# Kernel tuning notes

Measured on AMD Instinct MI355X. Metric: run time of the kernel, lower is better.

The kernel has to match this reference:

```python
import jax, jax.numpy as jnp
import numpy as np

B, N = 2, 6
FC, FH, FW = 256, 32, 88            # encoder feature shape
ORFH, ORFW = 256, 704               # original image H, W
OUT_C = 128
D_ST, D_END, D_STEP = 1.0, 60.0, 3.0
NXV, NYV, NZV = 256, 256, 1         # BEV voxel grid (x, y, z)
DXV = np.array([0.4, 0.4, 20.0], np.float32)          # dx
BXV = np.array([-51.0, -51.0, 0.0], np.float32)       # bx = bound_lo + dx/2
BN_EPS = 1e-3


def _conv(x, w, b):
    y = jax.lax.conv_general_dilated(x, w, (1, 1), 'SAME',
                                     dimension_numbers=('NCHW', 'OIHW', 'NCHW'))
    return y + b[None, :, None, None]


def _bn(x, scale, bias, mean, var):
    inv = scale / jnp.sqrt(var + BN_EPS)
    return x * inv[None, :, None, None] + (bias - mean * inv)[None, :, None, None]


def _frustum():
    ds = jnp.arange(D_ST, D_END, D_STEP, dtype=jnp.float32)      # (D,)
    xs = jnp.linspace(0.0, ORFW - 1.0, FW)
    ys = jnp.linspace(0.0, ORFH - 1.0, FH)
    f = jnp.stack(jnp.broadcast_arrays(xs[None, None, :], ys[None, :, None],
                                       ds[:, None, None]), axis=-1)  # (D,FH,FW,3)
    return f, ds


def _forward(cam2ego_rot, cam2ego_trans, cam_intrins, post_cam2ego_rot,
             post_cam2ego_trans, img_feats,
             conv1_w, conv1_b, bn1_s, bn1_b, bn1_m, bn1_v,
             conv2_w, conv2_b, bn2_s, bn2_b, bn2_m, bn2_v,
             conv3_w, conv3_b):
    frustum, depth_vals = _frustum()
    D = depth_vals.shape[0]
    # ---- geometry (GaussianLSS.get_geometry) ----
    pts = frustum[None, None] - post_cam2ego_trans[:, :, None, None, None, :]
    inv_post = jnp.linalg.inv(post_cam2ego_rot)                       # (B,N,3,3)
    pts = jnp.einsum('bnij,bndhwj->bndhwi', inv_post, pts)
    pts = jnp.concatenate([pts[..., :2] * pts[..., 2:3], pts[..., 2:3]], -1)
    combine = cam2ego_rot @ jnp.linalg.inv(cam_intrins)
    geometry = (jnp.einsum('bnij,bndhwj->bndhwi', combine, pts)
                + cam2ego_trans[:, :, None, None, None, :])           # (B,N,D,H,W,3)
    # ---- depth net + gaussian depth distribution (get_cam_feature) ----
    x = img_feats.reshape(B * N, FC, FH, FW)
    x = jax.nn.relu(_bn(_conv(x, conv1_w, conv1_b), bn1_s, bn1_b, bn1_m, bn1_v))
    x = jax.nn.relu(_bn(_conv(x, conv2_w, conv2_b), bn2_s, bn2_b, bn2_m, bn2_v))
    x = _conv(x, conv3_w, conv3_b)                                    # (BN, OUT_C+2, H, W)
    mu, log_sigma, feats = x[:, 0], x[:, 1], x[:, 2:]
    sigma = jnp.exp(log_sigma) + 1e-6
    g = jnp.exp(-0.5 * (depth_vals[None, :, None, None] - mu[:, None]) ** 2
                / (sigma[:, None] ** 2))                              # (BN,D,H,W)
    g = g / (jnp.sum(g, axis=1, keepdims=True) + 1e-6)
    vol = g[:, None] * feats[:, :, None]                              # (BN,C,D,H,W)
    vol = vol.reshape(B, N, OUT_C, D, FH, FW).transpose(0, 1, 3, 4, 5, 2)  # (B,N,D,H,W,C)
    # ---- bev_pool: voxelize + scatter-add ----
    dx = jnp.asarray(DXV)
    bx = jnp.asarray(BXV)
    geom = ((geometry - (bx - dx / 2.0)) / dx).astype(jnp.int32)      # trunc like .long()
    gx, gy, gz = geom[..., 0], geom[..., 1], geom[..., 2]
    kept = ((gx >= 0) & (gx < NXV) & (gy >= 0) & (gy < NYV)
            & (gz >= 0) & (gz < NZV))                                 # (B,N,D,H,W)
    bidx = jnp.arange(B, dtype=jnp.int32)[:, None, None, None, None]
    flat = ((bidx * NZV + gz) * NXV + gx) * NYV + gy
    flat = jnp.where(kept, flat, 0)
    w = kept.astype(vol.dtype)
    data = (vol * w[..., None]).reshape(-1, OUT_C)
    bev = jax.ops.segment_sum(data, flat.reshape(-1),
                              num_segments=B * NZV * NXV * NYV)
    # torch: (B,C,Z,X,Y) -> cat(unbind(dim=2), 1) -> (B, Z*C, X, Y)
    bev = bev.reshape(B, NZV, NXV, NYV, OUT_C).transpose(0, 1, 4, 2, 3)
    bev = bev.reshape(B, NZV * OUT_C, NXV, NYV)
    # ---- ref_bev_pool mask ----
    counts = jax.ops.segment_sum(w.reshape(-1), flat.reshape(-1),
                                 num_segments=B * NZV * NXV * NYV)
    mask = jnp.any(counts.reshape(B, NZV, NXV, NYV) > 0, axis=1)      # (B,X,Y) bool
    return bev, mask


def setup_inputs() -> dict:
    key = jax.random.key(0)
    ks = jax.random.split(key, 16)
    # camera->ego rotation: cam z -> ego x, cam x -> -ego y, cam y -> -ego z
    R = jnp.array([[0., 0., 1.], [-1., 0., 0.], [0., -1., 0.]], jnp.float32)
    cam2ego_rot = jnp.tile(R, (B, N, 1, 1)) + 0.01 * jax.random.normal(ks[0], (B, N, 3, 3))
    cam2ego_trans = jax.random.uniform(ks[1], (B, N, 3), minval=-2.0, maxval=2.0)
    K = jnp.array([[500., 0., ORFW / 2.], [0., 500., ORFH / 2.], [0., 0., 1.]], jnp.float32)
    cam_intrins = jnp.tile(K, (B, N, 1, 1))
    post_cam2ego_rot = jnp.tile(jnp.eye(3, dtype=jnp.float32), (B, N, 1, 1)) \
        + 0.005 * jax.random.normal(ks[2], (B, N, 3, 3))
    post_cam2ego_trans = 0.5 * jax.random.normal(ks[3], (B, N, 3))
    img_feats = 0.1 * jax.random.normal(ks[4], (B, N, FC, FH, FW))
    conv3_b = jnp.zeros((OUT_C + 2,)).at[0].set(25.0).at[1].set(2.3)  # mu~25m, sigma~10m
    return dict(
        cam2ego_rot=cam2ego_rot, cam2ego_trans=cam2ego_trans,
        cam_intrins=cam_intrins, post_cam2ego_rot=post_cam2ego_rot,
        post_cam2ego_trans=post_cam2ego_trans, img_feats=img_feats,
        conv1_w=0.02 * jax.random.normal(ks[5], (FC, FC, 3, 3)),
        conv1_b=jnp.zeros((FC,)),
        bn1_s=1.0 + 0.01 * jax.random.normal(ks[6], (FC,)),
        bn1_b=0.01 * jax.random.normal(ks[7], (FC,)),
        bn1_m=0.01 * jax.random.normal(ks[8], (FC,)),
        bn1_v=1.0 + 0.1 * jax.random.uniform(ks[9], (FC,)),
        conv2_w=0.02 * jax.random.normal(ks[10], (FC, FC, 3, 3)),
        conv2_b=jnp.zeros((FC,)),
        bn2_s=1.0 + 0.01 * jax.random.normal(ks[11], (FC,)),
        bn2_b=0.01 * jax.random.normal(ks[12], (FC,)),
        bn2_m=0.01 * jax.random.normal(ks[13], (FC,)),
        bn2_v=1.0 + 0.1 * jax.random.uniform(ks[14], (FC,)),
        conv3_w=0.02 * jax.random.normal(ks[15], (OUT_C + 2, FC, 1, 1)),
        conv3_b=conv3_b,
    )


def reference(cam2ego_rot, cam2ego_trans, cam_intrins, post_cam2ego_rot,
              post_cam2ego_trans, img_feats,
              conv1_w, conv1_b, bn1_s, bn1_b, bn1_m, bn1_v,
              conv2_w, conv2_b, bn2_s, bn2_b, bn2_m, bn2_v,
              conv3_w, conv3_b):
    return _forward(cam2ego_rot, cam2ego_trans, cam_intrins, post_cam2ego_rot,
                    post_cam2ego_trans, img_feats,
                    conv1_w, conv1_b, bn1_s, bn1_b, bn1_m, bn1_v,
                    conv2_w, conv2_b, bn2_s, bn2_b, bn2_m, bn2_v,
                    conv3_w, conv3_b)
```

## Files before the change

### kernel.cpp

```cpp
#include <hip/hip_runtime.h>
#include <math.h>

typedef unsigned short ushort_t;
typedef unsigned int uint_t;

#define NIMG 12
#define NCH  256
#define FH   32
#define FW   88
#define NPIX 2816
#define NDEP 20
#define NOUTC 128
#define NVOX 65536
#define NPTS 675840
#define NKEY 131072
#define NGP  33792
#define BEV_FLOATS 16777216u

#define B_OCC    0u
#define B_A1     4096u
#define B_C1     5120u
#define B_A2     6144u
#define B_C2     7168u
#define B_TOT    278528u
#define B_FEAT   282624u
#define B_RECS   17584128u
#define B_BEV    22990848u
#define B_VCODE  22990848u
#define B_WT     25694208u
#define B_CNT    28397568u
#define B_OFFS   28921856u
#define B_CUR    29446144u
#define B_SPINE  29970432u
#define B_XBF    29972480u
#define B_ACT1   47273984u
#define B_ACT2   64575488u
#define B_WSWZ1  81876992u
#define B_WSWZ2  83056640u
#define B_WSWZ3  84236288u

#define PREP_W2    2304
#define PREP_W3    4608
#define PREP_BN    4752
#define PREP_CAST0 4753
#define PREP_GEOM0 5281
#define PREP_NBLK  7921

#define GS_SCAN0   528
#define GS_NBLK    1040

typedef __attribute__((ext_vector_type(8))) short bf16x8;
typedef __attribute__((ext_vector_type(4))) float floatx4;
typedef __attribute__((ext_vector_type(4))) uint_t u32x4;

__device__ __forceinline__ ushort_t f2bf(float f) {
    uint_t x = __float_as_uint(f);
    return (ushort_t)((x + 0x7fffu + ((x >> 16) & 1u)) >> 16);
}
__device__ __forceinline__ float bf2f(ushort_t u) {
    return __uint_as_float(((uint_t)u) << 16);
}

__device__ __forceinline__ void inv3x3(const float* __restrict__ M, float* __restrict__ o) {
    float a=M[0],b=M[1],c=M[2],d=M[3],e=M[4],f=M[5],g=M[6],h=M[7],i=M[8];
    float A = e*i - f*h;
    float B = c*h - b*i;
    float C = b*f - c*e;
    float D = f*g - d*i;
    float E = a*i - c*g;
    float F = c*d - a*f;
    float G = d*h - e*g;
    float H = b*g - a*h;
    float I = a*e - b*d;
    float det = a*A + b*D + c*G;
    float id = 1.0f / det;
    o[0]=A*id; o[1]=B*id; o[2]=C*id;
    o[3]=D*id; o[4]=E*id; o[5]=F*id;
    o[6]=G*id; o[7]=H*id; o[8]=I*id;
}

__device__ __forceinline__ void wprep_one(
    const float* __restrict__ w, ushort_t* __restrict__ dst,
    int ntap, int ncib, int ncog, int nco, int nci, int idx, bool split)
{
    int j = idx & 7;
    int l = (idx >> 3) & 63;
    int pairidx = idx >> 9;
    int g = pairidx % ncog;
    int b = (pairidx / ncog) % ncib;
    int t = pairidx / (ncog * ncib);
    int co = g * 16 + (l & 15);
    int ci = b * 32 + (l >> 4) * 8 + j;
    float v = 0.0f;
    if (co < nco) v = w[((size_t)co * nci + ci) * ntap + t];
    ushort_t hi = f2bf(v);
    if (split) {
        dst[(size_t)pairidx * 1024 + l * 8 + j]       = hi;
        dst[(size_t)pairidx * 1024 + 512 + l * 8 + j] = f2bf(v - bf2f(hi));
    } else {
        dst[(size_t)pairidx * 512 + l * 8 + j] = hi;
    }
}

__global__ __launch_bounds__(256) void prep_all_kernel(
    const float* __restrict__ w1, ushort_t* __restrict__ d1,
    const float* __restrict__ w2, ushort_t* __restrict__ d2,
    const float* __restrict__ w3, ushort_t* __restrict__ d3,
    const float* __restrict__ c2e_rot, const float* __restrict__ c2e_trans,
    const float* __restrict__ intrins, const float* __restrict__ post_rot,
    const float* __restrict__ post_trans,
    const float* __restrict__ c1b, const float* __restrict__ s1,
    const float* __restrict__ bb1, const float* __restrict__ m1, const float* __restrict__ v1,
    const float* __restrict__ c2b, const float* __restrict__ s2,
    const float* __restrict__ bb2, const float* __restrict__ m2, const float* __restrict__ v2,
    float* __restrict__ A1, float* __restrict__ C1,
    float* __restrict__ A2, float* __restrict__ C2,
    const float* __restrict__ img_in, ushort_t* __restrict__ xbf_out,
    int* __restrict__ vcode, uint_t* __restrict__ cnt)
{
    __shared__ __align__(16) ushort_t clds[64 * 264];
    int bid = blockIdx.x;
    int t = threadIdx.x;
    if (bid < PREP_W2) {
        wprep_one(w1, d1, 9, 8, 16, 256, 256, bid * 256 + t, false);
    } else if (bid < PREP_W3) {
        wprep_one(w2, d2, 9, 8, 16, 256, 256, (bid - PREP_W2) * 256 + t, false);
    } else if (bid < PREP_BN) {
        int idx = (bid - PREP_W3) * 256 + t;
        if (idx < 36864) wprep_one(w3, d3, 1, 8, 9, 130, 256, idx, true);
    } else if (bid == PREP_BN) {
        float i1 = s1[t] / sqrtf(v1[t] + 1e-3f);
        A1[t] = i1;
        C1[t] = (c1b[t] - m1[t]) * i1 + bb1[t];
        float i2 = s2[t] / sqrtf(v2[t] + 1e-3f);
        A2[t] = i2;
        C2[t] = (c2b[t] - m2[t]) * i2 + bb2[t];
    } else if (bid < PREP_GEOM0) {
        int cblk = bid - PREP_CAST0;
        int img = cblk / 44;
        int px0 = (cblk - img * 44) * 64;
        const float* src = img_in + (size_t)img * NCH * NPIX;
        int pxl = t & 63;
        int cib = t >> 6;
        #pragma unroll 4
        for (int cc = 0; cc < 64; ++cc) {
            int ci = cc * 4 + cib;
            float v = src[(size_t)ci * NPIX + px0 + pxl];
            clds[pxl * 264 + ci] = f2bf(v);
        }
        __syncthreads();
        int wv = t >> 6, lane = t & 63;
        uint2* outv = (uint2*)xbf_out;
        #pragma unroll
        for (int i = 0; i < 16; ++i) {
            int p = wv * 16 + i;
            uint2 val = *(const uint2*)&clds[p * 264 + lane * 4];
            outv[(size_t)(img * NPIX + px0 + p) * 64 + lane] = val;
        }
    } else {
        int i = (bid - PREP_GEOM0) * 256 + t;
        int lane = t & 63;
        int hw  = i % NPIX;
        int tmp = i / NPIX;
        int d   = tmp % NDEP;
        int bn  = tmp / NDEP;
        int h = hw / FW, w = hw - h * FW;
        float ip[9], ki[9], comb[9];
        inv3x3(post_rot + bn * 9, ip);
        inv3x3(intrins  + bn * 9, ki);
        const float* R = c2e_rot + bn * 9;
        #pragma unroll
        for (int r = 0; r < 3; ++r)
            #pragma unroll
            for (int cc = 0; cc < 3; ++cc)
                comb[r*3+cc] = R[r*3+0]*ki[0*3+cc] + R[r*3+1]*ki[1*3+cc] + R[r*3+2]*ki[2*3+cc];
        float xs = (float)w * (703.0f / 87.0f);
        float ys = (float)h * (255.0f / 31.0f);
        float dv = 1.0f + 3.0f * (float)d;
        float fx = xs - post_trans[bn*3+0];
        float fy = ys - post_trans[bn*3+1];
        float fz = dv - post_trans[bn*3+2];
        float p0 = ip[0]*fx + ip[1]*fy + ip[2]*fz;
        float p1 = ip[3]*fx + ip[4]*fy + ip[5]*fz;
        float p2 = ip[6]*fx + ip[7]*fy + ip[8]*fz;
        p0 *= p2; p1 *= p2;
        float gx = comb[0]*p0 + comb[1]*p1 + comb[2]*p2 + c2e_trans[bn*3+0];
        float gy = comb[3]*p0 + comb[4]*p1 + comb[5]*p2 + c2e_trans[bn*3+1];
        float gz = comb[6]*p0 + comb[7]*p1 + comb[8]*p2 + c2e_trans[bn*3+2];
        const float cx = -51.0f - 0.2f, cy = -51.0f - 0.2f, cz = 0.0f - 10.0f;
        int ix = (int)((gx - cx) / 0.4f);
        int iy = (int)((gy - cy) / 0.4f);
        int iz = (int)((gz - cz) / 20.0f);
        bool kept = (ix >= 0) && (ix < 256) && (iy >= 0) && (iy < 256) && (iz == 0);
        int code = kept ? ((ix << 8) | iy) : -1;
        vcode[i] = code;

        int b = bn / 6;
        uint_t key = kept ? (uint_t)((b << 16) | code) : 0xFFFFFFFFu;
        uint_t prevkey = __shfl_up(key, 1);
        bool leader = (lane == 0) || (key != prevkey);
        unsigned long long mask = __ballot(leader);
        if (leader && kept) {
            unsigned long long higher = mask & ~((2ULL << lane) - 1ULL);
            int nxt = higher ? (__ffsll((long long)higher) - 1) : 64;
            atomicAdd(&cnt[key], (uint_t)(nxt - lane));
        }
    }
}

__global__ __launch_bounds__(256, 3) void conv3x3_mfma(
    const ushort_t* __restrict__ in,
    const ushort_t* __restrict__ wswz,
    const float* __restrict__ Abn, const float* __restrict__ Cbn,
    ushort_t* __restrict__ out)
{
    __shared__ __align__(16) ushort_t lds[2][8640];
    int bx = blockIdx.x;
    int cg = blockIdx.y;
    int img = bx >> 5, h = bx & 31;
    int t = threadIdx.x;
    int w = t >> 6, l = t & 63;
    int q = l >> 4, c = l & 15;
    const int n0s[6] = {0, 16, 32, 48, 64, 72};

    for (int i = t; i < 8640; i += 256) ((uint_t*)lds)[i] = 0;

    const u32x4* src4 = (const u32x4*)(in + (size_t)img * NPIX * 256);
    const bf16x8* wsA = (const bf16x8*)wswz;

    int gbase[5], loff[5];
    bool sval[5];
    #pragma unroll
    for (int k = 0; k < 5; ++k) {
        int p = t + k * 256;
        bool valid = (p < 1056);
        int chunk = p >> 2, sub = p & 3;
        int r = chunk / 88;
        int col = chunk - r * 88;
        int hin = h - 1 + r;
        bool inb = valid && (hin >= 0) && (hin < FH);
        sval[k] = inb;
        gbase[k] = inb ? ((hin * 88 + col) * 32 + sub) : 0;
        int cs = col + 1;
        int slot = sub ^ ((cs >> 1) & 3);
        loff[k] = ((r * 90 + cs) * 4 + slot) * 8;
    }

    floatx4 acc[2][6];
    #pragma unroll
    for (int m = 0; m < 2; ++m)
        #pragma unroll
        for (int n = 0; n < 6; ++n)
            acc[m][n] = (floatx4){0.f, 0.f, 0.f, 0.f};

    int g0 = cg * 8 + w * 2;

    __syncthreads();
    #pragma unroll
    for (int k = 0; k < 5; ++k)
        if (sval[k]) *(u32x4*)&lds[0][loff[k]] = src4[gbase[k]];

    int buf = 0;
    for (int kb = 0; kb < 8; ++kb) {
        __syncthreads();
        u32x4 sreg[5];
        if (kb < 7) {
            #pragma unroll
            for (int k = 0; k < 5; ++k)
                if (sval[k]) sreg[k] = src4[gbase[k] + (kb + 1) * 4];
        }
        const bf16x8* B = (const bf16x8*)lds[buf];

        bf16x8 a0, a1;
        {
            int pa = (0 * 8 + kb) * 16;
            a0 = wsA[(size_t)(pa + g0    ) * 64 + l];
            a1 = wsA[(size_t)(pa + g0 + 1) * 64 + l];
        }
        #pragma unroll
        for (int t9 = 0; t9 < 9; ++t9) {
            bf16x8 na0, na1;
            if (t9 < 8) {
                int pa = ((t9 + 1) * 8 + kb) * 16;
                na0 = wsA[(size_t)(pa + g0    ) * 64 + l];
                na1 = wsA[(size_t)(pa + g0 + 1) * 64 + l];
            }
            int ky = t9 / 3, kx = t9 - ky * 3;
            #pragma unroll
            for (int n = 0; n < 6; ++n) {
                int col = n0s[n] + kx + c;
                int slot = q ^ ((col >> 1) & 3);
                bf16x8 b = B[(ky * 90 + col) * 4 + slot];
                acc[0][n] = __builtin_amdgcn_mfma_f32_16x16x32_bf16(a0, b, acc[0][n], 0, 0, 0);
                acc[1][n] = __builtin_amdgcn_mfma_f32_16x16x32_bf16(a1, b, acc[1][n], 0, 0, 0);
            }
            if (t9 < 8) { a0 = na0; a1 = na1; }
        }
        if (kb < 7) {
            #pragma unroll
            for (int k = 0; k < 5; ++k)
                if (sval[k]) *(u32x4*)&lds[buf ^ 1][loff[k]] = sreg[k];
        }
        buf ^= 1;
    }

    #pragma unroll
    for (int m = 0; m < 2; ++m) {
        int cob = cg * 128 + w * 32 + m * 16 + q * 4;
        float ba0 = Abn[cob+0], ba1 = Abn[cob+1], ba2 = Abn[cob+2], ba3 = Abn[cob+3];
        float bc0 = Cbn[cob+0], bc1 = Cbn[cob+1], bc2 = Cbn[cob+2], bc3 = Cbn[cob+3];
        #pragma unroll
        for (int n = 0; n < 6; ++n) {
            if (n == 5 && c < 8) continue;
            int col = n0s[n] + c;
            floatx4 v = acc[m][n];
            uint_t lo = (uint_t)f2bf(fmaxf(v[0]*ba0+bc0, 0.f)) | ((uint_t)f2bf(fmaxf(v[1]*ba1+bc1, 0.f)) << 16);
            uint_t hi = (uint_t)f2bf(fmaxf(v[2]*ba2+bc2, 0.f)) | ((uint_t)f2bf(fmaxf(v[3]*ba3+bc3, 0.f)) << 16);
            uint2 val; val.x = lo; val.y = hi;
            *(uint2*)&out[((size_t)img * NPIX + h * 88 + col) * 256 + cob] = val;
        }
    }
}

__global__ __launch_bounds__(256, 4) void gemm_scan_kernel(
    const ushort_t* __restrict__ act2,
    const ushort_t* __restrict__ wswz3,
    const float* __restrict__ b3,
    ushort_t* __restrict__ feat, float* __restrict__ wt,
    const uint_t* __restrict__ cnt, uint_t* __restrict__ offs,
    uint_t* __restrict__ spine)
{
    __shared__ uint_t s[256];
    int t = threadIdx.x;
    if (blockIdx.x >= GS_SCAN0) {
        int blk = blockIdx.x - GS_SCAN0;
        int i = blk * 256 + t;
        uint_t v = cnt[i];
        s[t] = v;
        __syncthreads();
        #pragma unroll
        for (int off = 1; off < 256; off <<= 1) {
            uint_t add = (t >= off) ? s[t - off] : 0u;
            __syncthreads();
            s[t] += add;
            __syncthreads();
        }
        offs[i] = s[t] - v;
        if (t == 255) spine[blk] = s[255];
        return;
    }
    int wv = t >> 6, l = t & 63, q = l >> 4, c = l & 15;
    int n0 = (blockIdx.x * 4 + wv) * 16;
    int px = n0 + c;
    const bf16x8* A = (const bf16x8*)wswz3;
    const bf16x8* B = (const bf16x8*)act2;
    floatx4 acc[9];
    #pragma unroll
    for (int g = 0; g < 9; ++g) acc[g] = (floatx4){0.f, 0.f, 0.f, 0.f};
    for (int kb = 0; kb < 8; ++kb) {
        bf16x8 b = B[(size_t)px * 32 + kb * 4 + q];
        #pragma unroll
        for (int g = 0; g < 9; ++g) {
            size_t pa = (size_t)(kb * 9 + g) * 128;
            acc[g] = __builtin_amdgcn_mfma_f32_16x16x32_bf16(A[pa + l],      b, acc[g], 0, 0, 0);
            acc[g] = __builtin_amdgcn_mfma_f32_16x16x32_bf16(A[pa + 64 + l], b, acc[g], 0, 0, 0);
        }
    }
    #pragma unroll
    for (int g = 0; g < 9; ++g) {
        #pragma unroll
        for (int r = 0; r < 4; ++r) {
            int co = g * 16 + q * 4 + r;
            if (co < 2 || co >= 130) continue;
            feat[(size_t)px * 128 + (co - 2)] = f2bf(acc[g][r] + b3[co]);
        }
    }
    float muv = acc[0][0] + b3[0];
    float lsv = acc[0][1] + b3[1];
    float mu_b  = __shfl(muv, c);
    float sig   = expf(__shfl(lsv, c)) + 1e-6f;
    float ninv2 = -0.5f / (sig * sig);
    float g5[5]; float sum = 0.0f;
    #pragma unroll
    for (int j = 0; j < 5; ++j) {
        float dv = 1.0f + 3.0f * (float)(q * 5 + j);
        float df = dv - mu_b;
        g5[j] = expf(df * df * ninv2);
        sum += g5[j];
    }
    sum += __shfl_xor(sum, 16);
    sum += __shfl_xor(sum, 32);
    float inv = 1.0f / (sum + 1e-6f);
    #pragma unroll
    for (int j = 0; j < 5; ++j)
        wt[(size_t)(q * 5 + j) * NGP + px] = g5[j] * inv;
}

__global__ __launch_bounds__(256) void fixup_kernel(
    uint_t* __restrict__ offs, const uint_t* __restrict__ spine,
    uint_t* __restrict__ cursor, const uint_t* __restrict__ cnt,
    float* __restrict__ mask_out, uint_t* __restrict__ total,
    unsigned char* __restrict__ occ)
{
    __shared__ uint_t red[256];
    int bid = blockIdx.x, t = threadIdx.x;
    uint_t part = 0;
    for (int j = t; j < bid; j += 256) part += spine[j];
    red[t] = part;
    __syncthreads();
    #pragma unroll
    for (int off = 128; off > 0; off >>= 1) {
        if (t < off) red[t] += red[t + off];
        __syncthreads();
    }
    uint_t prefix = red[0];
    int i = bid * 256 + t;
    uint_t o = offs[i] + prefix;
    offs[i] = o;
    cursor[i] = o;
    uint_t n = cnt[i];
    mask_out[i] = (n > 0) ? 1.0f : 0.0f;
    int lane = t & 63, wv = t >> 6;
    unsigned long long any = __ballot(n > 0u);
    if (lane == 0) occ[bid * 4 + wv] = any ? 1 : 0;
    if (i == NKEY - 1) *total = o + n;
}

__global__ __launch_bounds__(256) void scatter_kernel(
    const int* __restrict__ vcode, const float* __restrict__ wt,
    uint_t* __restrict__ cursor, uint2* __restrict__ recs)
{
    int i = blockIdx.x * 256 + threadIdx.x;
    int lane = threadIdx.x & 63;
    int code = vcode[i];
    int hw  = i % NPIX;
    int tmp = i / NPIX;
    int d   = tmp % NDEP;
    int bn  = tmp / NDEP;
    int b   = bn / 6;
    int gp  = bn * NPIX + hw;
    bool active = (code >= 0);
    uint_t key = active ? (uint_t)((b << 16) | code) : 0xFFFFFFFFu;
    uint2 r;
    r.x = ((uint_t)(code & 0xffff) << 16) | (uint_t)gp;
    r.y = active ? __float_as_uint(wt[(size_t)d * NGP + gp]) : 0u;

    uint_t prevkey = __shfl_up(key, 1);
    bool leader = (lane == 0) || (key != prevkey);
    unsigned long long mask = __ballot(leader);
    uint_t base = 0;
    if (leader && active) {
        unsigned long long higher = mask & ~((2ULL << lane) - 1ULL);
        int nxt = higher ? (__ffsll((long long)higher) - 1) : 64;
        base = atomicAdd(&cursor[key], (uint_t)(nxt - lane));
    }
    unsigned long long lower = mask & ((2ULL << lane) - 1ULL);
    int lead = 63 - __clzll((long long)lower);
    base = __shfl(base, lead);
    if (active) recs[base + (lane - lead)] = r;
}

__global__ __launch_bounds__(256) void segreduce_kernel(
    const uint2* __restrict__ recs, const uint_t* __restrict__ total,
    const uint_t* __restrict__ featu,
    float* __restrict__ bev_tmp)
{
    uint_t R = *total;
    int wid = blockIdx.x * 4 + (threadIdx.x >> 6);
    uint_t start = (uint_t)wid * 64u;
    if (start >= R) return;
    int lane = threadIdx.x & 63;
    uint_t ustart = __builtin_amdgcn_readfirstlane(start);

    uint_t myidx = ustart + (uint_t)lane;
    if (myidx >= R) myidx = R - 1u;
    uint2 mr = recs[myidx];

    uint_t rx0 = (uint_t)__shfl((int)mr.x, 0);
    uint_t gp00 = rx0 & 0xffffu;
    uint_t prevk = ((gp00 >= 16896u) ? 0x10000u : 0u) | (rx0 >> 16);
    float acc0 = 0.f, acc1 = 0.f;

    uint_t fbuf[2][16];
    #pragma unroll
    for (int j = 0; j < 16; ++j) {
        uint_t rx = (uint_t)__shfl((int)mr.x, j);
        fbuf[0][j] = featu[(size_t)(rx & 0xffffu) * 64 + lane];
    }
    #pragma unroll
    for (int b = 0; b < 4; ++b) {
        if (b < 3) {
            #pragma unroll
            for (int j = 0; j < 16; ++j) {
                uint_t rx = (uint_t)__shfl((int)mr.x, (b + 1) * 16 + j);
                fbuf[(b + 1) & 1][j] = featu[(size_t)(rx & 0xffffu) * 64 + lane];
            }
        }
        #pragma unroll
        for (int j = 0; j < 16; ++j) {
            int e = b * 16 + j;
            uint_t rx = (uint_t)__shfl((int)mr.x, e);
            uint_t ry = (uint_t)__shfl((int)mr.y, e);
            uint_t gp = rx & 0xffffu;
            uint_t key = ((gp >= 16896u) ? 0x10000u : 0u) | (rx >> 16);
            float wv = __uint_as_float(ry);
            if (ustart + (uint_t)e >= R) { key = prevk; wv = 0.f; }
            if (key != prevk) {
                float* p = bev_tmp + (size_t)prevk * NOUTC;
                atomicAdd(p + 2 * lane,     acc0);
                atomicAdd(p + 2 * lane + 1, acc1);
                acc0 = acc1 = 0.f;
                prevk = key;
            }
            uint_t fv = fbuf[b & 1][j];
            acc0 = fmaf(wv, bf2f((ushort_t)(fv & 0xffffu)), acc0);
            acc1 = fmaf(wv, bf2f((ushort_t)(fv >> 16)),     acc1);
        }
    }
    float* p = bev_tmp + (size_t)prevk * NOUTC;
    atomicAdd(p + 2 * lane,     acc0);
    atomicAdd(p + 2 * lane + 1, acc1);
}

__global__ __launch_bounds__(256) void transpose_kernel(
    const float* __restrict__ bev_tmp, const unsigned char* __restrict__ occ,
    float* __restrict__ bev_out)
{
    __shared__ float lds[64 * 129];
    int blk = blockIdx.x;
    int b   = blk >> 10;
    int v0  = (blk & 1023) * 64;
    int t   = threadIdx.x;
    float* dst = bev_out + (size_t)b * NOUTC * NVOX + v0;
    if (!occ[blk]) {
        #pragma unroll
        for (int k = 0; k < 32; ++k) {
            int idx = k * 256 + t;
            int vl = idx & 63, ch = idx >> 6;
            dst[(size_t)ch * NVOX + vl] = 0.0f;
        }
        return;
    }
    const float* src = bev_tmp + ((size_t)b * NVOX + v0) * NOUTC;
    #pragma unroll
    for (int k = 0; k < 32; ++k) {
        int idx = k * 256 + t;
        int v = idx >> 7, ch = idx & 127;
        lds[v * 129 + ch] = src[idx];
    }
    __syncthreads();
    #pragma unroll
    for (int k = 0; k < 32; ++k) {
        int idx = k * 256 + t;
        int vl = idx & 63, ch = idx >> 6;
        dst[(size_t)ch * NVOX + vl] = lds[vl * 129 + ch];
    }
}

extern "C" void kernel_launch(void* const* d_in, const int* in_sizes, int n_in,
                              void* d_out, int out_size, void* d_ws, size_t ws_size,
                              hipStream_t stream) {
    const float* c2e_rot    = (const float*)d_in[0];
    const float* c2e_trans  = (const float*)d_in[1];
    const float* intrins    = (const float*)d_in[2];
    const float* post_rot   = (const float*)d_in[3];
    const float* post_trans = (const float*)d_in[4];
    const float* img_feats  = (const float*)d_in[5];
    const float* conv1_w    = (const float*)d_in[6];
    const float* conv1_b    = (const float*)d_in[7];
    const float* bn1_s = (const float*)d_in[8];
    const float* bn1_b = (const float*)d_in[9];
    const float* bn1_m = (const float*)d_in[10];
    const float* bn1_v = (const float*)d_in[11];
    const float* conv2_w = (const float*)d_in[12];
    const float* conv2_b = (const float*)d_in[13];
    const float* bn2_s = (const float*)d_in[14];
    const float* bn2_b = (const float*)d_in[15];
    const float* bn2_m = (const float*)d_in[16];
    const float* bn2_v = (const float*)d_in[17];
    const float* conv3_w = (const float*)d_in[18];
    const float* conv3_b = (const float*)d_in[19];

    char* base = (char*)d_ws;
    unsigned char* occ = (unsigned char*)(base + B_OCC);
    float*    A1     = (float*)(base + B_A1);
    float*    C1     = (float*)(base + B_C1);
    float*    A2     = (float*)(base + B_A2);
    float*    C2     = (float*)(base + B_C2);
    uint_t*   total  = (uint_t*)(base + B_TOT);
    ushort_t* feat   = (ushort_t*)(base + B_FEAT);
    uint2*    recs   = (uint2*)(base + B_RECS);
    float*    bevtmp = (float*)(base + B_BEV);
    int*      vcode  = (int*)(base + B_VCODE);
    float*    wt     = (float*)(base + B_WT);
    uint_t*   cnt    = (uint_t*)(base + B_CNT);
    uint_t*   offs   = (uint_t*)(base + B_OFFS);
    uint_t*   cursor = (uint_t*)(base + B_CUR);
    uint_t*   spine  = (uint_t*)(base + B_SPINE);
    ushort_t* xbf    = (ushort_t*)(base + B_XBF);
    ushort_t* act1   = (ushort_t*)(base + B_ACT1);
    ushort_t* act2   = (ushort_t*)(base + B_ACT2);
    ushort_t* wswz1  = (ushort_t*)(base + B_WSWZ1);
    ushort_t* wswz2  = (ushort_t*)(base + B_WSWZ2);
    ushort_t* wswz3  = (ushort_t*)(base + B_WSWZ3);

    float* bev_out  = (float*)d_out;
    float* mask_out = bev_out + BEV_FLOATS;

    hipMemsetAsync(cnt, 0, NKEY * sizeof(uint_t), stream);
    prep_all_kernel<<<PREP_NBLK, 256, 0, stream>>>(
        conv1_w, wswz1, conv2_w, wswz2, conv3_w, wswz3,
        c2e_rot, c2e_trans, intrins, post_rot, post_trans,
        conv1_b, bn1_s, bn1_b, bn1_m, bn1_v,
        conv2_b, bn2_s, bn2_b, bn2_m, bn2_v,
        A1, C1, A2, C2,
        img_feats, xbf, vcode, cnt);
    conv3x3_mfma<<<dim3(NIMG * 32, 2), 256, 0, stream>>>(xbf,  wswz1, A1, C1, act1);
    conv3x3_mfma<<<dim3(NIMG * 32, 2), 256, 0, stream>>>(act1, wswz2, A2, C2, act2);
    gemm_scan_kernel<<<GS_NBLK, 256, 0, stream>>>(act2, wswz3, conv3_b, feat, wt,
                                                  cnt, offs, spine);
    fixup_kernel<<<NKEY / 256, 256, 0, stream>>>(offs, spine, cursor, cnt, mask_out, total, occ);
    scatter_kernel<<<NPTS / 256, 256, 0, stream>>>(vcode, wt, cursor, recs);
    hipMemsetAsync(bevtmp, 0, (size_t)BEV_FLOATS * sizeof(float), stream);
    segreduce_kernel<<<(NPTS / 64 + 3) / 4, 256, 0, stream>>>(recs, total, (const uint_t*)feat, bevtmp);
    transpose_kernel<<<2048, 256, 0, stream>>>(bevtmp, occ, bev_out);
}
```

Measured before the change: 343.9 us.

## Make segment reduce owner-writes to drop bev memset and atomics

Each wave now processes only the segments that begin inside its 64-record chunk and continues past the chunk boundary to finish the last segment. This lets it write each voxel's result with a plain float2 store instead of atomics. The 64MB memset of the temporary BEV buffer is removed, and the transpose uses the occupancy mask to zero voxels that were never written. Workspace buffers are moved so that vcode and the counters no longer alias the BEV region. The cost is extra work when segments are long, and correctness depends on the mask exactly matching which voxels were written.

Measured after the change: 375.0 us. +9.0%, slower.

```diff
diff --git a/kernel.cpp b/kernel.cpp
--- a/kernel.cpp
+++ b/kernel.cpp
@@ -24,14 +24,14 @@
 #define B_C2     7168u
 #define B_TOT    278528u
 #define B_FEAT   282624u
+#define B_VCODE  8933376u
+#define B_WT     11636736u
+#define B_CNT    14340096u
+#define B_OFFS   14864384u
+#define B_CUR    15388672u
+#define B_SPINE  15912960u
 #define B_RECS   17584128u
 #define B_BEV    22990848u
-#define B_VCODE  22990848u
-#define B_WT     25694208u
-#define B_CNT    28397568u
-#define B_OFFS   28921856u
-#define B_CUR    29446144u
-#define B_SPINE  29970432u
 #define B_XBF    29972480u
 #define B_ACT1   47273984u
 #define B_ACT2   64575488u
@@ -473,12 +473,27 @@
     uint_t ustart = __builtin_amdgcn_readfirstlane(start);
 
     uint_t myidx = ustart + (uint_t)lane;
-    if (myidx >= R) myidx = R - 1u;
+    bool oob = (myidx >= R);
+    if (oob) myidx = R - 1u;
     uint2 mr = recs[myidx];
 
-    uint_t rx0 = (uint_t)__shfl((int)mr.x, 0);
-    uint_t gp00 = rx0 & 0xffffu;
-    uint_t prevk = ((gp00 >= 16896u) ? 0x10000u : 0u) | (rx0 >> 16);
+    uint_t mygp  = mr.x & 0xffffu;
+    uint_t mykey = ((mygp >= 16896u) ? 0x10000u : 0u) | (mr.x >> 16);
+
+    uint_t kprev = 0xFFFFFFFFu;
+    if (ustart > 0u) {
+        uint2 pr = recs[ustart - 1u];
+        uint_t pgp = pr.x & 0xffffu;
+        kprev = ((pgp >= 16896u) ? 0x10000u : 0u) | (pr.x >> 16);
+    }
+    uint_t upkey = (uint_t)__shfl_up((int)mykey, 1);
+    if (lane == 0) upkey = kprev;
+    bool strans = (!oob) && (mykey != upkey);
+    unsigned long long smask = __ballot(strans);
+    if (smask == 0ULL) return;
+    int s0 = __ffsll((long long)smask) - 1;
+
+    uint_t prevk = (uint_t)__shfl((int)mykey, s0);
     float acc0 = 0.f, acc1 = 0.f;
 
     uint_t fbuf[2][16];
@@ -504,11 +519,12 @@
             uint_t gp = rx & 0xffffu;
             uint_t key = ((gp >= 16896u) ? 0x10000u : 0u) | (rx >> 16);
             float wv = __uint_as_float(ry);
+            if (e < s0) continue;
             if (ustart + (uint_t)e >= R) { key = prevk; wv = 0.f; }
             if (key != prevk) {
                 float* p = bev_tmp + (size_t)prevk * NOUTC;
-                atomicAdd(p + 2 * lane,     acc0);
-                atomicAdd(p + 2 * lane + 1, acc1);
+                float2 st; st.x = acc0; st.y = acc1;
+                *(float2*)(p + 2 * lane) = st;
                 acc0 = acc1 = 0.f;
                 prevk = key;
             }
@@ -517,16 +533,53 @@
             acc1 = fmaf(wv, bf2f((ushort_t)(fv >> 16)),     acc1);
         }
     }
-    float* p = bev_tmp + (size_t)prevk * NOUTC;
-    atomicAdd(p + 2 * lane,     acc0);
-    atomicAdd(p + 2 * lane + 1, acc1);
+
+    uint_t cont = ustart + 64u;
+    while (cont < R) {
+        uint_t ci = cont + (uint_t)lane;
+        bool coob = (ci >= R);
+        uint2 cr = recs[coob ? (R - 1u) : ci];
+        uint_t cgp  = cr.x & 0xffffu;
+        uint_t ckey = ((cgp >= 16896u) ? 0x10000u : 0u) | (cr.x >> 16);
+        bool stop = coob || (ckey != prevk);
+        unsigned long long stopm = __ballot(stop);
+        int t1 = stopm ? (__ffsll((long long)stopm) - 1) : 64;
+        #pragma unroll
+        for (int sb = 0; sb < 4; ++sb) {
+            if (sb * 16 >= t1) break;
+            uint_t cf[16];
+            #pragma unroll
+            for (int j = 0; j < 16; ++j) {
+                uint_t rx = (uint_t)__shfl((int)cr.x, sb * 16 + j);
+                cf[j] = featu[(size_t)(rx & 0xffffu) * 64 + lane];
+            }
+            #pragma unroll
+            for (int j = 0; j < 16; ++j) {
+                int e = sb * 16 + j;
+                if (e >= t1) break;
+                uint_t ry = (uint_t)__shfl((int)cr.y, e);
+                float wv = __uint_as_float(ry);
+                uint_t fv = cf[j];
+                acc0 = fmaf(wv, bf2f((ushort_t)(fv & 0xffffu)), acc0);
+                acc1 = fmaf(wv, bf2f((ushort_t)(fv >> 16)),     acc1);
+            }
+        }
+        if (t1 < 64) break;
+        cont += 64u;
+    }
+    {
+        float* p = bev_tmp + (size_t)prevk * NOUTC;
+        float2 st; st.x = acc0; st.y = acc1;
+        *(float2*)(p + 2 * lane) = st;
+    }
 }
 
 __global__ __launch_bounds__(256) void transpose_kernel(
     const float* __restrict__ bev_tmp, const unsigned char* __restrict__ occ,
-    float* __restrict__ bev_out)
+    const float* __restrict__ mask, float* __restrict__ bev_out)
 {
     __shared__ float lds[64 * 129];
+    __shared__ float lmask[64];
     int blk = blockIdx.x;
     int b   = blk >> 10;
     int v0  = (blk & 1023) * 64;
@@ -541,12 +594,14 @@
         }
         return;
     }
+    if (t < 64) lmask[t] = mask[(size_t)b * NVOX + v0 + t];
+    __syncthreads();
     const float* src = bev_tmp + ((size_t)b * NVOX + v0) * NOUTC;
     #pragma unroll
     for (int k = 0; k < 32; ++k) {
         int idx = k * 256 + t;
         int v = idx >> 7, ch = idx & 127;
-        lds[v * 129 + ch] = src[idx];
+        lds[v * 129 + ch] = (lmask[v] != 0.0f) ? src[idx] : 0.0f;
     }
     __syncthreads();
     #pragma unroll
@@ -621,7 +676,6 @@
                                                   cnt, offs, spine);
     fixup_kernel<<<NKEY / 256, 256, 0, stream>>>(offs, spine, cursor, cnt, mask_out, total, occ);
     scatter_kernel<<<NPTS / 256, 256, 0, stream>>>(vcode, wt, cursor, recs);
-    hipMemsetAsync(bevtmp, 0, (size_t)BEV_FLOATS * sizeof(float), stream);
     segreduce_kernel<<<(NPTS / 64 + 3) / 4, 256, 0, stream>>>(recs, total, (const uint_t*)feat, bevtmp);
-    transpose_kernel<<<2048, 256, 0, stream>>>(bevtmp, occ, bev_out);
-}
+    transpose_kernel<<<2048, 256, 0, stream>>>(bevtmp, occ, mask_out, bev_out);
+}
```
